# Optimization experiments

Hardware: AMD Instinct MI355X
Metric: run time of the kernel (lower is better)

## Reference

```python
import jax, jax.numpy as jnp
import numpy as np

N = 100000      # nodes
E = 400000      # edges
F_IN = 602      # Reddit features
H = 256         # hidden
C = 42          # classes


def setup_inputs() -> dict:
    key = jax.random.key(0)
    ks = jax.random.split(key, 8)
    x = jax.random.normal(ks[0], (N, F_IN), dtype=jnp.float32)
    edge_index = jax.random.randint(ks[1], (2, E), 0, N, dtype=jnp.int32)
    s1 = 1.0 / np.sqrt(F_IN)
    s2 = 1.0 / np.sqrt(H)
    return {
        "x": x,
        "edge_index": edge_index,
        # layer 1 (SAGEConv: lin_l on aggregated neighbors w/ bias, lin_r on root no bias)
        "Wl1": jax.random.uniform(ks[2], (F_IN, H), jnp.float32, -s1, s1),
        "bl1": jnp.zeros((H,), jnp.float32),
        "Wr1": jax.random.uniform(ks[3], (F_IN, H), jnp.float32, -s1, s1),
        # layer 2
        "Wl2": jax.random.uniform(ks[4], (H, C), jnp.float32, -s2, s2),
        "bl2": jnp.zeros((C,), jnp.float32),
        "Wr2": jax.random.uniform(ks[5], (H, C), jnp.float32, -s2, s2),
    }


def _sage_conv(x, src, dst, Wl, bl, Wr, num_nodes):
    # gather source features along edges, mean-aggregate per destination node
    msgs = x[src]                                               # [E, F]
    summed = jax.ops.segment_sum(msgs, dst, num_segments=num_nodes)  # [N, F]
    cnt = jax.ops.segment_sum(jnp.ones((src.shape[0], 1), x.dtype), dst,
                              num_segments=num_nodes)           # [N, 1]
    mean = summed / jnp.maximum(cnt, 1.0)                       # isolated nodes -> 0
    return mean @ Wl + bl + x @ Wr


def reference(x, edge_index, Wl1, bl1, Wr1, Wl2, bl2, Wr2):
    src, dst = edge_index[0], edge_index[1]
    n = x.shape[0]
    h = jax.nn.relu(_sage_conv(x, src, dst, Wl1, bl1, Wr1, n))
    # dropout is identity in eval mode
    out = _sage_conv(h, src, dst, Wl2, bl2, Wr2, n)
    return jax.nn.log_softmax(out, axis=1)
```

## Files before the change

### kernel.cpp

```cpp
#include <hip/hip_runtime.h>
#include <stdint.h>

#define NN 100000
#define NE 400000
#define FIN 602
#define HID 256
#define NC 42
#define NB_SCAN 98

typedef __attribute__((ext_vector_type(8))) short bf16x8;
typedef __attribute__((ext_vector_type(4))) float f32x4;
typedef __attribute__((ext_vector_type(2))) float f32x2;
typedef __attribute__((ext_vector_type(4))) short s16x4;

static __device__ __forceinline__ short f2bf(float f) {
  union { float f; uint32_t u; } v; v.f = f;
  uint32_t r = (v.u + 0x7fffu + ((v.u >> 16) & 1u)) >> 16;
  return (short)(uint16_t)r;
}
static __device__ __forceinline__ float bf2f(short s) {
  union { uint32_t u; float f; } v; v.u = ((uint32_t)(uint16_t)s) << 16;
  return v.f;
}
static __device__ __forceinline__ uint32_t cvtpk(float a, float b) {
  uint32_t r;
  asm("v_cvt_pk_bf16_f32 %0, %1, %2" : "=v"(r) : "v"(a), "v"(b));
  return r;
}
static __device__ __forceinline__ bf16x8 pack8(f32x2 a, f32x2 b, f32x2 c, f32x2 d) {
  union { bf16x8 v; uint32_t u[4]; } r;
  r.u[0] = cvtpk(a[0], a[1]);
  r.u[1] = cvtpk(b[0], b[1]);
  r.u[2] = cvtpk(c[0], c[1]);
  r.u[3] = cvtpk(d[0], d[1]);
  return r.v;
}

__global__ __launch_bounds__(256) void k_count(const int* __restrict__ dst, int* __restrict__ cnt) {
  int t = blockIdx.x * 256 + threadIdx.x;
  if (t < NE) atomicAdd(&cnt[dst[t]], 1);
}

__global__ __launch_bounds__(1024) void k_scan_local(const int* __restrict__ cnt, int* __restrict__ rowptr,
                                                     int* __restrict__ bsum) {
  __shared__ int sm[1024];
  int tid = threadIdx.x, t = blockIdx.x * 1024 + tid;
  int v = (t < NN) ? cnt[t] : 0;
  sm[tid] = v;
  __syncthreads();
  for (int off = 1; off < 1024; off <<= 1) {
    int y = (tid >= off) ? sm[tid - off] : 0;
    __syncthreads();
    sm[tid] += y;
    __syncthreads();
  }
  if (t < NN) rowptr[t] = sm[tid] - v;
  if (tid == 1023) bsum[blockIdx.x] = sm[tid];
}
__global__ __launch_bounds__(128) void k_scan_bsum(int* __restrict__ bsum) {
  __shared__ int sm[128];
  int tid = threadIdx.x;
  int v = (tid < NB_SCAN) ? bsum[tid] : 0;
  sm[tid] = v;
  __syncthreads();
  for (int off = 1; off < 128; off <<= 1) {
    int y = (tid >= off) ? sm[tid - off] : 0;
    __syncthreads();
    sm[tid] += y;
    __syncthreads();
  }
  if (tid < NB_SCAN) bsum[tid] = sm[tid] - v;
}
__global__ __launch_bounds__(1024) void k_scan_add(int* __restrict__ rowptr, const int* __restrict__ bsum) {
  int t = blockIdx.x * 1024 + threadIdx.x;
  if (t < NN) rowptr[t] += bsum[t >> 10];
  if (t == 0) rowptr[NN] = NE;
}

__global__ __launch_bounds__(256) void k_sort(const int* __restrict__ src, const int* __restrict__ dst,
                                              const int* __restrict__ rowptr, int* __restrict__ epos,
                                              int* __restrict__ esorted) {
  int t = blockIdx.x * 256 + threadIdx.x;
  if (t >= NE) return;
  int d = dst[t];
  int p = atomicAdd(&epos[d], 1);
  esorted[rowptr[d] + p] = src[t];
}

__global__ __launch_bounds__(256) void k_prep_w1(const float* __restrict__ Wl, const float* __restrict__ Wr,
                                                 short* __restrict__ wf) {
  int idx = blockIdx.x * 256 + threadIdx.x;
  if (idx >= 32 * 19 * 512) return;
  int i = idx & 7, l = (idx >> 3) & 63, rest = idx >> 9;
  int ks = rest % 19, ct = rest / 19;
  int c = ct * 16 + (l & 15);
  int k = ks * 32 + ((l >> 4) << 3) + i;
  float v = 0.f;
  if (k < FIN) v = (c < HID) ? Wl[k * HID + c] : Wr[k * HID + (c - HID)];
  wf[idx] = f2bf(v);
}
__global__ __launch_bounds__(256) void k_prep_w2(const float* __restrict__ Wl, const float* __restrict__ Wr,
                                                 short* __restrict__ wf) {
  int idx = blockIdx.x * 256 + threadIdx.x;
  if (idx >= 6 * 8 * 512) return;
  int i = idx & 7, l = (idx >> 3) & 63, rest = idx >> 9;
  int ks = rest & 7, ct = rest >> 3;
  int c = ct * 16 + (l & 15);
  int k = ks * 32 + ((l >> 4) << 3) + i;
  float v = 0.f;
  if (c < NC) v = Wl[k * NC + c];
  else if (c < 2 * NC) v = Wr[k * NC + (c - NC)];
  wf[idx] = f2bf(v);
}

__global__ __launch_bounds__(256) void k_gemm_l1(const float* __restrict__ x, const short* __restrict__ wf,
                                                 short* __restrict__ t1, short* __restrict__ t2) {
  const int lane = threadIdx.x & 63;
  const int w = threadIdx.x >> 6;
  const int lr = lane & 15, lg = lane >> 4;
  const int row0 = blockIdx.x * 32;

  f32x4 acc[2][8];
#pragma unroll
  for (int a = 0; a < 2; ++a)
#pragma unroll
    for (int b = 0; b < 8; ++b)
      acc[a][b] = (f32x4){0.f, 0.f, 0.f, 0.f};

  const float* xr0 = x + (size_t)(row0 + lr) * FIN + lg * 8;
  const float* xr1 = xr0 + (size_t)16 * FIN;
  const short* wbL = wf + (size_t)(w * 4) * 19 * 512 + lane * 8;
  const short* wbR = wf + (size_t)(16 + w * 4) * 19 * 512 + lane * 8;

  f32x2 xb[2][8];
#pragma unroll
  for (int i = 0; i < 4; ++i) {
    xb[0][i]     = *(const f32x2*)(xr0 + 2 * i);
    xb[0][4 + i] = *(const f32x2*)(xr1 + 2 * i);
  }

#pragma unroll
  for (int ks = 0; ks < 18; ++ks) {
    const int cur = ks & 1, nxt = cur ^ 1;
    bf16x8 bbL[4], bbR[4];
#pragma unroll
    for (int c = 0; c < 4; ++c) bbL[c] = *(const bf16x8*)(wbL + (size_t)(c * 19 + ks) * 512);
#pragma unroll
    for (int c = 0; c < 4; ++c) bbR[c] = *(const bf16x8*)(wbR + (size_t)(c * 19 + ks) * 512);
    if (ks < 17) {
      const float* p0 = xr0 + (ks + 1) * 32;
      const float* p1 = xr1 + (ks + 1) * 32;
#pragma unroll
      for (int i = 0; i < 4; ++i) {
        xb[nxt][i]     = *(const f32x2*)(p0 + 2 * i);
        xb[nxt][4 + i] = *(const f32x2*)(p1 + 2 * i);
      }
    }
    bf16x8 a0 = pack8(xb[cur][0], xb[cur][1], xb[cur][2], xb[cur][3]);
    bf16x8 a1 = pack8(xb[cur][4], xb[cur][5], xb[cur][6], xb[cur][7]);
#pragma unroll
    for (int c = 0; c < 4; ++c) {
      acc[0][c]     = __builtin_amdgcn_mfma_f32_16x16x32_bf16(a0, bbL[c], acc[0][c], 0, 0, 0);
      acc[1][c]     = __builtin_amdgcn_mfma_f32_16x16x32_bf16(a1, bbL[c], acc[1][c], 0, 0, 0);
      acc[0][4 + c] = __builtin_amdgcn_mfma_f32_16x16x32_bf16(a0, bbR[c], acc[0][4 + c], 0, 0, 0);
      acc[1][4 + c] = __builtin_amdgcn_mfma_f32_16x16x32_bf16(a1, bbR[c], acc[1][4 + c], 0, 0, 0);
    }
  }
  {
    const float* p0 = xr0 + 576;
    const float* p1 = xr1 + 576;
    bf16x8 a0, a1;
#pragma unroll
    for (int i = 0; i < 8; ++i) {
      bool ok = (576 + lg * 8 + i) < FIN;
      a0[i] = ok ? f2bf(p0[i]) : (short)0;
      a1[i] = ok ? f2bf(p1[i]) : (short)0;
    }
#pragma unroll
    for (int c = 0; c < 4; ++c) {
      bf16x8 bL = *(const bf16x8*)(wbL + (size_t)(c * 19 + 18) * 512);
      bf16x8 bR = *(const bf16x8*)(wbR + (size_t)(c * 19 + 18) * 512);
      acc[0][c]     = __builtin_amdgcn_mfma_f32_16x16x32_bf16(a0, bL, acc[0][c], 0, 0, 0);
      acc[1][c]     = __builtin_amdgcn_mfma_f32_16x16x32_bf16(a1, bL, acc[1][c], 0, 0, 0);
      acc[0][4 + c] = __builtin_amdgcn_mfma_f32_16x16x32_bf16(a0, bR, acc[0][4 + c], 0, 0, 0);
      acc[1][4 + c] = __builtin_amdgcn_mfma_f32_16x16x32_bf16(a1, bR, acc[1][4 + c], 0, 0, 0);
    }
  }
#pragma unroll
  for (int rt = 0; rt < 2; ++rt)
#pragma unroll
    for (int c = 0; c < 4; ++c)
#pragma unroll
      for (int j = 0; j < 4; ++j) {
        int row = row0 + rt * 16 + lg * 4 + j;
        int col = w * 64 + c * 16 + lr;
        t1[(size_t)row * HID + col] = f2bf(acc[rt][c][j]);
        t2[(size_t)row * HID + col] = f2bf(acc[rt][4 + c][j]);
      }
}

__global__ __launch_bounds__(256) void k_gather1(const short* __restrict__ t1, short* __restrict__ t2h,
                                                 const int* __restrict__ rowptr, const int* __restrict__ esorted,
                                                 const float* __restrict__ bl) {
  int t = blockIdx.x * 256 + threadIdx.x;
  int n = t >> 6, lane = t & 63;
  if (n >= NN) return;
  s16x4 tv = *(const s16x4*)(t2h + (size_t)n * HID + lane * 4);
  int beg = rowptr[n], end = rowptr[n + 1];
  float a0 = 0.f, a1 = 0.f, a2 = 0.f, a3 = 0.f;
  for (int j = beg; j < end; ++j) {
    int s = esorted[j];
    s16x4 v = *(const s16x4*)(t1 + (size_t)s * HID + lane * 4);
    a0 += bf2f(v[0]); a1 += bf2f(v[1]); a2 += bf2f(v[2]); a3 += bf2f(v[3]);
  }
  int deg = end - beg;
  float inv = 1.0f / (float)(deg > 1 ? deg : 1);
  f32x4 b = *(const f32x4*)(bl + lane * 4);
  s16x4 o;
  float v0 = a0 * inv + b[0] + bf2f(tv[0]);
  float v1 = a1 * inv + b[1] + bf2f(tv[1]);
  float v2 = a2 * inv + b[2] + bf2f(tv[2]);
  float v3 = a3 * inv + b[3] + bf2f(tv[3]);
  o[0] = f2bf(v0 > 0.f ? v0 : 0.f);
  o[1] = f2bf(v1 > 0.f ? v1 : 0.f);
  o[2] = f2bf(v2 > 0.f ? v2 : 0.f);
  o[3] = f2bf(v3 > 0.f ? v3 : 0.f);
  *(s16x4*)(t2h + (size_t)n * HID + lane * 4) = o;
}

__global__ __launch_bounds__(256) void k_gemm2(const short* __restrict__ h, const short* __restrict__ wf,
                                               float* __restrict__ u) {
  const int lane = threadIdx.x & 63;
  const int w = threadIdx.x >> 6;
  const int lr = lane & 15, lg = lane >> 4;
  const int row0 = blockIdx.x * 128 + w * 32;

  f32x4 acc[2][6];
#pragma unroll
  for (int a = 0; a < 2; ++a)
#pragma unroll
    for (int b = 0; b < 6; ++b)
      acc[a][b] = (f32x4){0.f, 0.f, 0.f, 0.f};

  const int r0 = row0 + lr, r1 = row0 + 16 + lr;
#pragma unroll
  for (int ks = 0; ks < 8; ++ks) {
    bf16x8 a0, a1;
#pragma unroll
    for (int i = 0; i < 8; ++i) { a0[i] = 0; a1[i] = 0; }
    if (r0 < NN) a0 = *(const bf16x8*)(h + (size_t)r0 * HID + ks * 32 + lg * 8);
    if (r1 < NN) a1 = *(const bf16x8*)(h + (size_t)r1 * HID + ks * 32 + lg * 8);
    bf16x8 bfrag[6];
#pragma unroll
    for (int ct = 0; ct < 6; ++ct)
      bfrag[ct] = *(const bf16x8*)(wf + (size_t)((ct * 8 + ks) * 64 + lane) * 8);
#pragma unroll
    for (int ct = 0; ct < 6; ++ct) {
      acc[0][ct] = __builtin_amdgcn_mfma_f32_16x16x32_bf16(a0, bfrag[ct], acc[0][ct], 0, 0, 0);
      acc[1][ct] = __builtin_amdgcn_mfma_f32_16x16x32_bf16(a1, bfrag[ct], acc[1][ct], 0, 0, 0);
    }
  }
#pragma unroll
  for (int rt = 0; rt < 2; ++rt)
#pragma unroll
    for (int ct = 0; ct < 6; ++ct)
#pragma unroll
      for (int j = 0; j < 4; ++j) {
        int row = row0 + rt * 16 + lg * 4 + j;
        int col = ct * 16 + lr;
        if (row < NN) u[(size_t)row * 96 + col] = acc[rt][ct][j];
      }
}

__global__ __launch_bounds__(256) void k_final(const float* __restrict__ u, const int* __restrict__ rowptr,
                                               const int* __restrict__ esorted, const float* __restrict__ bl,
                                               float* __restrict__ out) {
  int t = blockIdx.x * 256 + threadIdx.x;
  int n = t >> 6, c = t & 63;
  if (n >= NN) return;
  int beg = rowptr[n], end = rowptr[n + 1];
  float a = 0.f;
  if (c < NC) {
    for (int j = beg; j < end; ++j) {
      int s = esorted[j];
      a += u[(size_t)s * 96 + c];
    }
  }
  int deg = end - beg;
  float inv = 1.0f / (float)(deg > 1 ? deg : 1);
  float v = (c < NC) ? (a * inv + bl[c] + u[(size_t)n * 96 + NC + c]) : -1e30f;
  float m = v;
#pragma unroll
  for (int off = 32; off > 0; off >>= 1) m = fmaxf(m, __shfl_xor(m, off));
  float e = (c < NC) ? __expf(v - m) : 0.f;
#pragma unroll
  for (int off = 32; off > 0; off >>= 1) e += __shfl_xor(e, off);
  float lse = __logf(e);
  if (c < NC) out[(size_t)n * NC + c] = v - m - lse;
}

extern "C" void kernel_launch(void* const* d_in, const int* in_sizes, int n_in,
                              void* d_out, int out_size, void* d_ws, size_t ws_size,
                              hipStream_t stream) {
  const float* x   = (const float*)d_in[0];
  const int* eidx  = (const int*)d_in[1];
  const float* Wl1 = (const float*)d_in[2];
  const float* bl1 = (const float*)d_in[3];
  const float* Wr1 = (const float*)d_in[4];
  const float* Wl2 = (const float*)d_in[5];
  const float* bl2 = (const float*)d_in[6];
  const float* Wr2 = (const float*)d_in[7];
  float* out = (float*)d_out;
  const int* src = eidx;
  const int* dstp = eidx + NE;

  char* ws = (char*)d_ws;
  int*   cnt     = (int*)(ws + 0);
  int*   rowptr  = (int*)(ws + 524288);
  int*   epos    = (int*)(ws + 1048576);
  int*   bsum    = (int*)(ws + 1462272);
  short* wf1     = (short*)(ws + 1572864);
  short* wf2     = (short*)(ws + 2359296);
  int*   esorted = (int*)(ws + 2621440);
  short* t1      = (short*)(ws + 4300800);
  short* t2h     = (short*)(ws + 55500800);
  float* u       = (float*)(ws + 4300800);

  hipMemsetAsync(cnt, 0, (size_t)NN * sizeof(int), stream);
  hipMemsetAsync(epos, 0, (size_t)NN * sizeof(int), stream);
  k_prep_w1<<<(32 * 19 * 512 + 255) / 256, 256, 0, stream>>>(Wl1, Wr1, wf1);
  k_prep_w2<<<(6 * 8 * 512 + 255) / 256, 256, 0, stream>>>(Wl2, Wr2, wf2);
  k_count<<<(NE + 255) / 256, 256, 0, stream>>>(dstp, cnt);
  k_scan_local<<<NB_SCAN, 1024, 0, stream>>>(cnt, rowptr, bsum);
  k_scan_bsum<<<1, 128, 0, stream>>>(bsum);
  k_scan_add<<<NB_SCAN, 1024, 0, stream>>>(rowptr, bsum);
  k_sort<<<(NE + 255) / 256, 256, 0, stream>>>(src, dstp, rowptr, epos, esorted);
  k_gemm_l1<<<NN / 32, 256, 0, stream>>>(x, wf1, t1, t2h);
  k_gather1<<<(NN * 64) / 256, 256, 0, stream>>>(t1, t2h, rowptr, esorted, bl1);
  k_gemm2<<<(NN + 127) / 128, 256, 0, stream>>>(t2h, wf2, u);
  k_final<<<(NN * 64) / 256, 256, 0, stream>>>(u, rowptr, esorted, bl2, out);
}
```

Measured before the change: 776.0 us.

## Stage x tiles in swizzled LDS via global_load_lds with 64-row blocks

The layer-1 GEMM now stages x into a double-buffered, XOR-swizzled LDS tile using direct global-to-LDS loads, in place of per-lane register loads. Each block covers 64 rows instead of 32, so every wave reuses each loaded weight fragment across four row tiles and weight traffic per row is halved. The separate tail step for the last K slice is folded into the main loop by clamping out-of-range columns, which relies on the padded weights being zero. The cost is twice as many accumulator registers, a block barrier per K step, and lower occupancy.

New measurement: 708.2 us. -8.7%, faster.

```diff
diff --git a/kernel.cpp b/kernel.cpp
--- a/kernel.cpp
+++ b/kernel.cpp
@@ -27,13 +27,17 @@
   asm("v_cvt_pk_bf16_f32 %0, %1, %2" : "=v"(r) : "v"(a), "v"(b));
   return r;
 }
-static __device__ __forceinline__ bf16x8 pack8(f32x2 a, f32x2 b, f32x2 c, f32x2 d) {
+static __device__ __forceinline__ bf16x8 pack8q(f32x4 a, f32x4 b) {
   union { bf16x8 v; uint32_t u[4]; } r;
   r.u[0] = cvtpk(a[0], a[1]);
-  r.u[1] = cvtpk(b[0], b[1]);
-  r.u[2] = cvtpk(c[0], c[1]);
-  r.u[3] = cvtpk(d[0], d[1]);
+  r.u[1] = cvtpk(a[2], a[3]);
+  r.u[2] = cvtpk(b[0], b[1]);
+  r.u[3] = cvtpk(b[2], b[3]);
   return r.v;
+}
+static __device__ __forceinline__ void gload_lds4(const float* g, float* lds) {
+  __builtin_amdgcn_global_load_lds((const __attribute__((address_space(1))) void*)g,
+                                   (__attribute__((address_space(3))) void*)lds, 4, 0, 0);
 }
 
 __global__ __launch_bounds__(256) void k_count(const int* __restrict__ dst, int* __restrict__ cnt) {
@@ -115,87 +119,81 @@
 
 __global__ __launch_bounds__(256) void k_gemm_l1(const float* __restrict__ x, const short* __restrict__ wf,
                                                  short* __restrict__ t1, short* __restrict__ t2) {
+  __shared__ float xs[2][64 * 32];
   const int lane = threadIdx.x & 63;
   const int w = threadIdx.x >> 6;
   const int lr = lane & 15, lg = lane >> 4;
-  const int row0 = blockIdx.x * 32;
-
-  f32x4 acc[2][8];
-#pragma unroll
-  for (int a = 0; a < 2; ++a)
+  const int row0 = blockIdx.x * 64;
+
+  f32x4 acc[4][8];
+#pragma unroll
+  for (int a = 0; a < 4; ++a)
 #pragma unroll
     for (int b = 0; b < 8; ++b)
       acc[a][b] = (f32x4){0.f, 0.f, 0.f, 0.f};
 
-  const float* xr0 = x + (size_t)(row0 + lr) * FIN + lg * 8;
-  const float* xr1 = xr0 + (size_t)16 * FIN;
   const short* wbL = wf + (size_t)(w * 4) * 19 * 512 + lane * 8;
   const short* wbR = wf + (size_t)(16 + w * 4) * 19 * 512 + lane * 8;
 
-  f32x2 xb[2][8];
-#pragma unroll
-  for (int i = 0; i < 4; ++i) {
-    xb[0][i]     = *(const f32x2*)(xr0 + 2 * i);
-    xb[0][4 + i] = *(const f32x2*)(xr1 + 2 * i);
-  }
-
-#pragma unroll
-  for (int ks = 0; ks < 18; ++ks) {
-    const int cur = ks & 1, nxt = cur ^ 1;
+  const int s_rhalf = lane >> 5;
+  const int s_pq = (lane & 31) >> 2;
+  const int s_pe = lane & 3;
+
+#define STAGE(KS, BUF)                                                                   \
+  {                                                                                      \
+    _Pragma("unroll")                                                                    \
+    for (int q = 0; q < 8; ++q) {                                                        \
+      int r = w * 16 + 2 * q + s_rhalf;                                                  \
+      int rs = row0 + r; rs = rs < NN ? rs : NN - 1;                                     \
+      int ld = ((s_pq ^ (r & 7)) << 2) | s_pe;                                           \
+      int k = (KS) * 32 + ld;                                                            \
+      k = k < FIN ? k : 0;                                                               \
+      gload_lds4(x + (size_t)rs * FIN + k, &xs[BUF][(w * 16 + 2 * q) * 32]);             \
+    }                                                                                    \
+  }
+
+  STAGE(0, 0);
+  __syncthreads();
+
+  for (int ks = 0; ks < 19; ++ks) {
+    const int cur = ks & 1;
+    if (ks < 18) STAGE(ks + 1, cur ^ 1);
     bf16x8 bbL[4], bbR[4];
 #pragma unroll
     for (int c = 0; c < 4; ++c) bbL[c] = *(const bf16x8*)(wbL + (size_t)(c * 19 + ks) * 512);
 #pragma unroll
     for (int c = 0; c < 4; ++c) bbR[c] = *(const bf16x8*)(wbR + (size_t)(c * 19 + ks) * 512);
-    if (ks < 17) {
-      const float* p0 = xr0 + (ks + 1) * 32;
-      const float* p1 = xr1 + (ks + 1) * 32;
-#pragma unroll
-      for (int i = 0; i < 4; ++i) {
-        xb[nxt][i]     = *(const f32x2*)(p0 + 2 * i);
-        xb[nxt][4 + i] = *(const f32x2*)(p1 + 2 * i);
+    bf16x8 af[4];
+#pragma unroll
+    for (int t = 0; t < 4; ++t) {
+      const char* rowp = (const char*)&xs[cur][(t * 16 + lr) * 32];
+      f32x4 v0 = *(const f32x4*)(rowp + (((lg * 2 + 0) ^ (lr & 7)) << 4));
+      f32x4 v1 = *(const f32x4*)(rowp + (((lg * 2 + 1) ^ (lr & 7)) << 4));
+      af[t] = pack8q(v0, v1);
+    }
+#pragma unroll
+    for (int c = 0; c < 4; ++c)
+#pragma unroll
+      for (int t = 0; t < 4; ++t) {
+        acc[t][c]     = __builtin_amdgcn_mfma_f32_16x16x32_bf16(af[t], bbL[c], acc[t][c], 0, 0, 0);
+        acc[t][4 + c] = __builtin_amdgcn_mfma_f32_16x16x32_bf16(af[t], bbR[c], acc[t][4 + c], 0, 0, 0);
       }
-    }
-    bf16x8 a0 = pack8(xb[cur][0], xb[cur][1], xb[cur][2], xb[cur][3]);
-    bf16x8 a1 = pack8(xb[cur][4], xb[cur][5], xb[cur][6], xb[cur][7]);
-#pragma unroll
-    for (int c = 0; c < 4; ++c) {
-      acc[0][c]     = __builtin_amdgcn_mfma_f32_16x16x32_bf16(a0, bbL[c], acc[0][c], 0, 0, 0);
-      acc[1][c]     = __builtin_amdgcn_mfma_f32_16x16x32_bf16(a1, bbL[c], acc[1][c], 0, 0, 0);
-      acc[0][4 + c] = __builtin_amdgcn_mfma_f32_16x16x32_bf16(a0, bbR[c], acc[0][4 + c], 0, 0, 0);
-      acc[1][4 + c] = __builtin_amdgcn_mfma_f32_16x16x32_bf16(a1, bbR[c], acc[1][4 + c], 0, 0, 0);
-    }
-  }
-  {
-    const float* p0 = xr0 + 576;
-    const float* p1 = xr1 + 576;
-    bf16x8 a0, a1;
-#pragma unroll
-    for (int i = 0; i < 8; ++i) {
-      bool ok = (576 + lg * 8 + i) < FIN;
-      a0[i] = ok ? f2bf(p0[i]) : (short)0;
-      a1[i] = ok ? f2bf(p1[i]) : (short)0;
-    }
-#pragma unroll
-    for (int c = 0; c < 4; ++c) {
-      bf16x8 bL = *(const bf16x8*)(wbL + (size_t)(c * 19 + 18) * 512);
-      bf16x8 bR = *(const bf16x8*)(wbR + (size_t)(c * 19 + 18) * 512);
-      acc[0][c]     = __builtin_amdgcn_mfma_f32_16x16x32_bf16(a0, bL, acc[0][c], 0, 0, 0);
-      acc[1][c]     = __builtin_amdgcn_mfma_f32_16x16x32_bf16(a1, bL, acc[1][c], 0, 0, 0);
-      acc[0][4 + c] = __builtin_amdgcn_mfma_f32_16x16x32_bf16(a0, bR, acc[0][4 + c], 0, 0, 0);
-      acc[1][4 + c] = __builtin_amdgcn_mfma_f32_16x16x32_bf16(a1, bR, acc[1][4 + c], 0, 0, 0);
-    }
-  }
-#pragma unroll
-  for (int rt = 0; rt < 2; ++rt)
-#pragma unroll
-    for (int c = 0; c < 4; ++c)
+    __syncthreads();
+  }
+#undef STAGE
+
+#pragma unroll
+  for (int t = 0; t < 4; ++t)
+#pragma unroll
+    for (int c = 0; c < 8; ++c)
 #pragma unroll
       for (int j = 0; j < 4; ++j) {
-        int row = row0 + rt * 16 + lg * 4 + j;
-        int col = w * 64 + c * 16 + lr;
-        t1[(size_t)row * HID + col] = f2bf(acc[rt][c][j]);
-        t2[(size_t)row * HID + col] = f2bf(acc[rt][4 + c][j]);
+        int row = row0 + t * 16 + lg * 4 + j;
+        if (row < NN) {
+          int col = w * 64 + (c & 3) * 16 + lr;
+          short* dstb = (c < 4) ? t1 : t2;
+          dstb[(size_t)row * HID + col] = f2bf(acc[t][c][j]);
+        }
       }
 }
 
@@ -335,7 +333,7 @@
   k_scan_bsum<<<1, 128, 0, stream>>>(bsum);
   k_scan_add<<<NB_SCAN, 1024, 0, stream>>>(rowptr, bsum);
   k_sort<<<(NE + 255) / 256, 256, 0, stream>>>(src, dstp, rowptr, epos, esorted);
-  k_gemm_l1<<<NN / 32, 256, 0, stream>>>(x, wf1, t1, t2h);
+  k_gemm_l1<<<(NN + 63) / 64, 256, 0, stream>>>(x, wf1, t1, t2h);
   k_gather1<<<(NN * 64) / 256, 256, 0, stream>>>(t1, t2h, rowptr, esorted, bl1);
   k_gemm2<<<(NN + 127) / 128, 256, 0, stream>>>(t2h, wf2, u);
   k_final<<<(NN * 64) / 256, 256, 0, stream>>>(u, rowptr, esorted, bl2, out);
```
